# Kernel optimization log

Measured on AMD Instinct MI355X. Metric: run time of the kernel, lower is better.

The kernel has to match this reference:

```python
import jax, jax.numpy as jnp
import numpy as np

B = 131072    # batch of toy 2D points
H = 256       # effective hidden width (dims[1], = out_dims * group_card)
NB = 8        # n_blocks i-ResBlocks
NMID = 3      # middle layers: dims 2->256->256->256->256->2 => 1 in + 3 mid + 1 out
NPS = 5       # n_power_series terms for log-det trace estimator


def setup_inputs() -> dict:
    key = jax.random.key(0)
    ks = jax.random.split(key, 8)
    # small scales keep each g-net contractive (coeff<1 Lipschitz, as spectral norm would)
    x  = jax.random.normal(ks[0], (B, 2), jnp.float32)
    v  = jax.random.normal(ks[1], (B, 2), jnp.float32)  # Hutchinson probe (n_samples=1)
    Wi = jax.random.normal(ks[2], (NB, 2, H), jnp.float32) * 0.05
    bi = jax.random.normal(ks[3], (NB, H), jnp.float32) * 0.01
    Wm = jax.random.normal(ks[4], (NB, NMID, H, H), jnp.float32) * (0.05 / np.sqrt(H))
    bm = jax.random.normal(ks[5], (NB, NMID, H), jnp.float32) * 0.01
    Wo = jax.random.normal(ks[6], (NB, H, 2), jnp.float32) * (0.05 / np.sqrt(H))
    bo = jax.random.normal(ks[7], (NB, 2), jnp.float32) * 0.01
    return {"x": x, "v": v, "Wi": Wi, "bi": bi, "Wm": Wm, "bm": bm, "Wo": Wo, "bo": bo}


def _g(x, Wi, bi, Wm, bm, Wo, bo):
    # equivariant 3x3 convs on 1x1 spatial maps == channel-mixing linears;
    # build_nnet appends the activation after EVERY conv, including the last.
    h = jax.nn.relu(x @ Wi + bi)
    for j in range(Wm.shape[0]):
        h = jax.nn.relu(h @ Wm[j] + bm[j])
    return jax.nn.relu(h @ Wo + bo)


def _iresblock(x, v, Wi, bi, Wm, bm, Wo, bo):
    gfun = lambda xx: _g(xx, Wi, bi, Wm, bm, Wo, bo)
    gx = gfun(x)
    # log det(I + J_g) ~= sum_{k=1..n} (-1)^{k+1}/k * v^T J_g^k v  (power series, Hutchinson)
    w = v
    logdet = jnp.zeros((x.shape[0], 1), x.dtype)
    for k in range(1, NPS + 1):
        _, w = jax.jvp(gfun, (x,), (w,))          # w <- J_g @ w
        coef = ((-1.0) ** (k + 1)) / k
        logdet = logdet + coef * jnp.sum(w * v, axis=1, keepdims=True)
    return x + gx, logdet


def reference(x, v, Wi, bi, Wm, bm, Wo, bo):
    z = x
    delta_logp = jnp.zeros((x.shape[0], 1), x.dtype)  # SequentialFlow: logpx - logdet per block
    for b in range(NB):
        z, ld = _iresblock(z, v, Wi[b], bi[b], Wm[b], bm[b], Wo[b], bo[b])
        delta_logp = delta_logp - ld
    return z, delta_logp
```

## Files before the change

kernel.cpp:

```cpp
#include <hip/hip_runtime.h>
#include <hip/hip_bf16.h>

#define BATCH 131072
#define H 256
#define NBLK 8
#define NMID 3
#define MS 32
#define RT_N 6
#define NT 256

typedef __attribute__((ext_vector_type(8))) short short8;
typedef __attribute__((ext_vector_type(4))) float f32x4;

__device__ __forceinline__ unsigned pk2(float a, float b) {
    unsigned ua = __float_as_uint(a) + 0x8000u;
    unsigned ub = __float_as_uint(b) + 0x8000u;
    return __builtin_amdgcn_perm(ub, ua, 0x07060302u);
}
__device__ __forceinline__ unsigned short f2bf(float f) {
    return (unsigned short)((__float_as_uint(f) + 0x8000u) >> 16);
}

__global__ void pack_w_kernel(const float* __restrict__ Wm, unsigned short* __restrict__ Wp) {
    int o = blockIdx.x * blockDim.x + threadIdx.x;
    if (o >= NBLK * NMID * 8192) return;
    int lane  = o & 63;
    int T     = (o >> 6) & 15;
    int kk    = (o >> 10) & 7;
    int layer = o >> 13;
    int n  = (T >> 2) * 64 + (lane & 15) * 4 + (T & 3);
    int k0 = kk * 32 + (lane >> 4) * 8;
    const float* src = Wm + (size_t)layer * H * H;
    unsigned int w[4];
    #pragma unroll
    for (int jj = 0; jj < 4; ++jj)
        w[jj] = pk2(src[(size_t)(k0 + 2*jj) * H + n], src[(size_t)(k0 + 2*jj + 1) * H + n]);
    uint4 val; val.x = w[0]; val.y = w[1]; val.z = w[2]; val.w = w[3];
    ((uint4*)Wp)[o] = val;
}

__device__ __forceinline__ void epilogue_write(const f32x4 (&acc)[RT_N][4],
                                               const float* __restrict__ bias,
                                               unsigned short* __restrict__ Xs,
                                               int wave, int lane) {
    const int mcol = lane & 15, quad = lane >> 4;
    const int nb = wave * 64 + mcol * 4;
    const float4 bv = *(const float4*)(bias + nb);
    const int kkx = nb >> 5;
    const int qx  = (nb >> 3) & 3;
    const int jb  = nb & 7;
    #pragma unroll
    for (int g = 0; g < 2; ++g) {
        #pragma unroll
        for (int r = 0; r < 4; ++r) {
            float pre[4], hv[4], ta[4], tb[4];
            pre[0] = acc[g][0][r] + bv.x; pre[1] = acc[g][1][r] + bv.y;
            pre[2] = acc[g][2][r] + bv.z; pre[3] = acc[g][3][r] + bv.w;
            #pragma unroll
            for (int c = 0; c < 4; ++c) {
                bool mk = pre[c] > 0.0f;
                hv[c] = mk ? pre[c]        : 0.0f;
                ta[c] = mk ? acc[2+g][c][r] : 0.0f;
                tb[c] = mk ? acc[4+g][c][r] : 0.0f;
            }
            int rowm = quad * 4 + r;
            int le   = qx * 16 + rowm;
            int scl  = le ^ ((le >> 3) & 7);
            int e0   = (((g * 8 + kkx) * 64 + scl) * 8) + jb;
            uint2 ph; ph.x = pk2(hv[0], hv[1]); ph.y = pk2(hv[2], hv[3]);
            uint2 pa; pa.x = pk2(ta[0], ta[1]); pa.y = pk2(ta[2], ta[3]);
            uint2 pb; pb.x = pk2(tb[0], tb[1]); pb.y = pk2(tb[2], tb[3]);
            *(uint2*)(Xs + e0)          = ph;
            *(uint2*)(Xs + e0 + 8192)   = pa;
            *(uint2*)(Xs + e0 + 16384)  = pb;
        }
    }
}

__global__ __launch_bounds__(NT, 2)
void flow_kernel(const float* __restrict__ x, const float* __restrict__ v,
                 const float* __restrict__ Wi, const float* __restrict__ bi,
                 const float* __restrict__ bm, const float* __restrict__ Wo,
                 const float* __restrict__ bo,
                 const unsigned short* __restrict__ Wp,
                 float* __restrict__ out)
{
    __shared__ uint4 Xl4[RT_N * 8 * 64];
    __shared__ float zbuf[MS * 2];
    __shared__ float vbuf[MS * 2];

    unsigned short* Xs = (unsigned short*)Xl4;

    const int tid  = threadIdx.x;
    const int wave = tid >> 6;
    const int lane = tid & 63;
    const int mcol = lane & 15;
    const int quad = lane >> 4;
    const int s0   = blockIdx.x * MS;
    const int rl   = lane ^ ((lane >> 3) & 7);

    float dlp = 0.0f;
    if (tid < MS) {
        zbuf[tid*2+0] = x[(size_t)(s0+tid)*2+0];
        zbuf[tid*2+1] = x[(size_t)(s0+tid)*2+1];
        vbuf[tid*2+0] = v[(size_t)(s0+tid)*2+0];
        vbuf[tid*2+1] = v[(size_t)(s0+tid)*2+1];
    }
    __syncthreads();

    for (int b = 0; b < NBLK; ++b) {
        #pragma unroll
        for (int cc = 0; cc < 2; ++cc) {
            int c = cc * NT + tid;
            if (c < 384) {
                int rt = c >> 6, cl = c & 63;
                int l = cl ^ ((cl >> 3) & 7);
                int m = l & 15, q = l >> 4;
                int st = rt >> 1;
                uint4 pk = {0u, 0u, 0u, 0u};
                if (q == 0) {
                    if (st == 0) {
                        int s = ((rt & 1) << 4) | m;
                        pk.x = pk2(zbuf[s*2+0], zbuf[s*2+1]);
                    } else if (st == 1) pk.x = 0x00003F80u;
                    else                pk.x = 0x3F800000u;
                }
                Xl4[rt * 512 + cl] = pk;
            }
        }
        __syncthreads();

        const float* Wi0 = Wi + (size_t)b * 2 * H;
        const float* Wi1 = Wi0 + H;
        {
            short8 b0[4];
            #pragma unroll
            for (int ct = 0; ct < 4; ++ct) {
                short8 z = {0,0,0,0,0,0,0,0};
                if (lane < 16) {
                    int n = wave * 64 + lane * 4 + ct;
                    unsigned p = pk2(Wi0[n], Wi1[n]);
                    z[0] = (short)(p & 0xFFFFu);
                    z[1] = (short)(p >> 16);
                }
                b0[ct] = z;
            }
            f32x4 acc[RT_N][4];
            #pragma unroll
            for (int rt = 0; rt < RT_N; ++rt)
                #pragma unroll
                for (int ct = 0; ct < 4; ++ct)
                    acc[rt][ct] = (f32x4){0.f, 0.f, 0.f, 0.f};
            #pragma unroll
            for (int rt = 0; rt < RT_N; ++rt) {
                short8 af = ((const short8*)Xl4)[(rt * 8) * 64 + rl];
                #pragma unroll
                for (int ct = 0; ct < 4; ++ct)
                    acc[rt][ct] = __builtin_amdgcn_mfma_f32_16x16x32_bf16(af, b0[ct], acc[rt][ct], 0, 0, 0);
            }
            __syncthreads();
            epilogue_write(acc, bi + (size_t)b * H, Xs, wave, lane);
            __syncthreads();
        }

        for (int li = 0; li < NMID; ++li) {
            const int layer = b * NMID + li;
            const short8* Bp  = ((const short8*)Wp) + (size_t)layer * 8192;
            const float* bias = bm + (size_t)layer * H;

            f32x4 acc[RT_N][4];
            #pragma unroll
            for (int rt = 0; rt < RT_N; ++rt)
                #pragma unroll
                for (int ct = 0; ct < 4; ++ct)
                    acc[rt][ct] = (f32x4){0.f, 0.f, 0.f, 0.f};

            #pragma unroll
            for (int kk = 0; kk < 8; ++kk) {
                short8 bf[4];
                #pragma unroll
                for (int ct = 0; ct < 4; ++ct)
                    bf[ct] = Bp[(kk*16 + wave*4 + ct)*64 + lane];
                #pragma unroll
                for (int rt = 0; rt < RT_N; ++rt) {
                    short8 af = ((const short8*)Xl4)[(rt*8 + kk)*64 + rl];
                    #pragma unroll
                    for (int ct = 0; ct < 4; ++ct)
                        acc[rt][ct] = __builtin_amdgcn_mfma_f32_16x16x32_bf16(af, bf[ct], acc[rt][ct], 0, 0, 0);
                }
            }
            __syncthreads();
            epilogue_write(acc, bias, Xs, wave, lane);
            __syncthreads();
        }

        const float* Wob = Wo + (size_t)b * H * 2;
        const float* bob = bo + (size_t)b * 2;
        {
            short8 b4[2];
            #pragma unroll
            for (int kki = 0; kki < 2; ++kki) {
                short8 z = {0,0,0,0,0,0,0,0};
                if (mcol < 2) {
                    int kb = (wave * 2 + kki) * 32 + quad * 8;
                    #pragma unroll
                    for (int jj = 0; jj < 4; ++jj) {
                        unsigned p = pk2(Wob[(kb + 2*jj) * 2 + mcol], Wob[(kb + 2*jj + 1) * 2 + mcol]);
                        z[2*jj]   = (short)(p & 0xFFFFu);
                        z[2*jj+1] = (short)(p >> 16);
                    }
                }
                b4[kki] = z;
            }
            f32x4 accL[RT_N];
            #pragma unroll
            for (int rt = 0; rt < RT_N; ++rt) accL[rt] = (f32x4){0.f, 0.f, 0.f, 0.f};
            #pragma unroll
            for (int rt = 0; rt < RT_N; ++rt) {
                short8 a0 = ((const short8*)Xl4)[(rt*8 + wave*2    )*64 + rl];
                accL[rt] = __builtin_amdgcn_mfma_f32_16x16x32_bf16(a0, b4[0], accL[rt], 0, 0, 0);
                short8 a1 = ((const short8*)Xl4)[(rt*8 + wave*2 + 1)*64 + rl];
                accL[rt] = __builtin_amdgcn_mfma_f32_16x16x32_bf16(a1, b4[1], accL[rt], 0, 0, 0);
            }
            __syncthreads();
            float* part = (float*)Xl4;
            if (mcol < 2) {
                #pragma unroll
                for (int rt = 0; rt < RT_N; ++rt)
                    #pragma unroll
                    for (int r = 0; r < 4; ++r)
                        part[((rt*16 + quad*4 + r)*2 + mcol)*4 + wave] = accL[rt][r];
            }
            __syncthreads();
            float* res = part + 768;
            if (tid < 192) {
                float4 p4 = ((const float4*)part)[tid];
                res[tid] = p4.x + p4.y + p4.z + p4.w;
            }
            __syncthreads();
            if (tid < MS) {
                int g = tid >> 4, row = tid & 15;
                int base = (g * 16 + row) * 2;
                float SH0 = res[base], SH1 = res[base + 1];
                float SA0 = res[base + 64], SA1 = res[base + 65];
                float SB0 = res[base + 128], SB1 = res[base + 129];
                float pre0 = SH0 + bob[0], pre1 = SH1 + bob[1];
                bool  m0 = pre0 > 0.f,     m1 = pre1 > 0.f;
                float gx0 = m0 ? pre0 : 0.f, gx1 = m1 ? pre1 : 0.f;
                float J00 = m0 ? SA0 : 0.f;
                float J01 = m0 ? SB0 : 0.f;
                float J10 = m1 ? SA1 : 0.f;
                float J11 = m1 ? SB1 : 0.f;
                float v0 = vbuf[tid*2+0], v1 = vbuf[tid*2+1];
                float w0 = v0, w1 = v1, ld = 0.f;
                const float coef[5] = {1.f, -0.5f, 1.f/3.f, -0.25f, 0.2f};
                #pragma unroll
                for (int k = 0; k < 5; ++k) {
                    float nw0 = fmaf(J00, w0, J01 * w1);
                    float nw1 = fmaf(J10, w0, J11 * w1);
                    w0 = nw0; w1 = nw1;
                    ld = fmaf(coef[k], fmaf(w0, v0, w1 * v1), ld);
                }
                zbuf[tid*2+0] += gx0;
                zbuf[tid*2+1] += gx1;
                dlp -= ld;
            }
        }
        __syncthreads();
    }

    if (tid < MS) {
        out[(size_t)(s0+tid)*2+0] = zbuf[tid*2+0];
        out[(size_t)(s0+tid)*2+1] = zbuf[tid*2+1];
        out[(size_t)2*BATCH + s0 + tid] = dlp;
    }
}

extern "C" void kernel_launch(void* const* d_in, const int* in_sizes, int n_in,
                              void* d_out, int out_size, void* d_ws, size_t ws_size,
                              hipStream_t stream) {
    const float* x  = (const float*)d_in[0];
    const float* v  = (const float*)d_in[1];
    const float* Wi = (const float*)d_in[2];
    const float* bi = (const float*)d_in[3];
    const float* Wm = (const float*)d_in[4];
    const float* bm = (const float*)d_in[5];
    const float* Wo = (const float*)d_in[6];
    const float* bo = (const float*)d_in[7];
    unsigned short* Wp = (unsigned short*)d_ws;

    int nchunks = NBLK * NMID * 8192;
    pack_w_kernel<<<(nchunks + 255) / 256, 256, 0, stream>>>(Wm, Wp);
    flow_kernel<<<BATCH / MS, NT, 0, stream>>>(x, v, Wi, bi, bm, Wo, bo, Wp, (float*)d_out);
}
```

Before: 1.261 ms.

## Split hidden columns across eight waves and build input-layer fragments in registers

Doubles the block size to 512 threads, so each wave computes 32 instead of 64 output columns per layer, halving per-wave MFMA work and accumulator registers. The weight packing layout and epilogue indexing change to match, and the reduction of the output layer now sums eight wave partials. The first layer's A fragments are now built directly from zbuf in registers instead of being staged through LDS, which removes one barrier per block. The middle-layer epilogue math runs before the barrier so it can overlap with other waves. The cost is more barrier participants and a larger cross-wave reduction, in exchange for lower register pressure and more waves in flight to hide latency.

```diff
diff --git a/kernel.cpp b/kernel.cpp
--- a/kernel.cpp
+++ b/kernel.cpp
@@ -7,7 +7,8 @@
 #define NMID 3
 #define MS 32
 #define RT_N 6
-#define NT 256
+#define NT 512
+#define CT_N 2
 
 typedef __attribute__((ext_vector_type(8))) short short8;
 typedef __attribute__((ext_vector_type(4))) float f32x4;
@@ -16,9 +17,6 @@
     unsigned ua = __float_as_uint(a) + 0x8000u;
     unsigned ub = __float_as_uint(b) + 0x8000u;
     return __builtin_amdgcn_perm(ub, ua, 0x07060302u);
-}
-__device__ __forceinline__ unsigned short f2bf(float f) {
-    return (unsigned short)((__float_as_uint(f) + 0x8000u) >> 16);
 }
 
 __global__ void pack_w_kernel(const float* __restrict__ Wm, unsigned short* __restrict__ Wp) {
@@ -28,7 +26,7 @@
     int T     = (o >> 6) & 15;
     int kk    = (o >> 10) & 7;
     int layer = o >> 13;
-    int n  = (T >> 2) * 64 + (lane & 15) * 4 + (T & 3);
+    int n  = (T >> 1) * 32 + (lane & 15) * 2 + (T & 1);
     int k0 = kk * 32 + (lane >> 4) * 8;
     const float* src = Wm + (size_t)layer * H * H;
     unsigned int w[4];
@@ -39,45 +37,44 @@
     ((uint4*)Wp)[o] = val;
 }
 
-__device__ __forceinline__ void epilogue_write(const f32x4 (&acc)[RT_N][4],
-                                               const float* __restrict__ bias,
-                                               unsigned short* __restrict__ Xs,
-                                               int wave, int lane) {
-    const int mcol = lane & 15, quad = lane >> 4;
-    const int nb = wave * 64 + mcol * 4;
-    const float4 bv = *(const float4*)(bias + nb);
-    const int kkx = nb >> 5;
-    const int qx  = (nb >> 3) & 3;
-    const int jb  = nb & 7;
+struct Packs { unsigned ph[2][4]; unsigned pa[2][4]; unsigned pb[2][4]; };
+
+__device__ __forceinline__ void epi_compute(const f32x4 (&acc)[RT_N][CT_N],
+                                            const float2 bv, Packs& p) {
     #pragma unroll
     for (int g = 0; g < 2; ++g) {
         #pragma unroll
         for (int r = 0; r < 4; ++r) {
-            float pre[4], hv[4], ta[4], tb[4];
-            pre[0] = acc[g][0][r] + bv.x; pre[1] = acc[g][1][r] + bv.y;
-            pre[2] = acc[g][2][r] + bv.z; pre[3] = acc[g][3][r] + bv.w;
-            #pragma unroll
-            for (int c = 0; c < 4; ++c) {
-                bool mk = pre[c] > 0.0f;
-                hv[c] = mk ? pre[c]        : 0.0f;
-                ta[c] = mk ? acc[2+g][c][r] : 0.0f;
-                tb[c] = mk ? acc[4+g][c][r] : 0.0f;
-            }
-            int rowm = quad * 4 + r;
-            int le   = qx * 16 + rowm;
-            int scl  = le ^ ((le >> 3) & 7);
-            int e0   = (((g * 8 + kkx) * 64 + scl) * 8) + jb;
-            uint2 ph; ph.x = pk2(hv[0], hv[1]); ph.y = pk2(hv[2], hv[3]);
-            uint2 pa; pa.x = pk2(ta[0], ta[1]); pa.y = pk2(ta[2], ta[3]);
-            uint2 pb; pb.x = pk2(tb[0], tb[1]); pb.y = pk2(tb[2], tb[3]);
-            *(uint2*)(Xs + e0)          = ph;
-            *(uint2*)(Xs + e0 + 8192)   = pa;
-            *(uint2*)(Xs + e0 + 16384)  = pb;
-        }
-    }
-}
-
-__global__ __launch_bounds__(NT, 2)
+            float c0 = acc[g][0][r] + bv.x;
+            float c1 = acc[g][1][r] + bv.y;
+            bool m0 = c0 > 0.0f, m1 = c1 > 0.0f;
+            p.ph[g][r] = pk2(m0 ? c0 : 0.0f,             m1 ? c1 : 0.0f);
+            p.pa[g][r] = pk2(m0 ? acc[2+g][0][r] : 0.0f, m1 ? acc[2+g][1][r] : 0.0f);
+            p.pb[g][r] = pk2(m0 ? acc[4+g][0][r] : 0.0f, m1 ? acc[4+g][1][r] : 0.0f);
+        }
+    }
+}
+
+__device__ __forceinline__ void epi_store(const Packs& p, unsigned short* __restrict__ Xs,
+                                          int wave, int lane) {
+    const int mcol = lane & 15, quad = lane >> 4;
+    const int qx = (mcol >> 2) & 3;
+    const int jb = (mcol & 3) * 2;
+    #pragma unroll
+    for (int g = 0; g < 2; ++g) {
+        #pragma unroll
+        for (int r = 0; r < 4; ++r) {
+            int le  = qx * 16 + quad * 4 + r;
+            int scl = le ^ ((le >> 3) & 7);
+            int e0  = ((g * 8 + wave) * 64 + scl) * 8 + jb;
+            *(unsigned*)(Xs + e0)         = p.ph[g][r];
+            *(unsigned*)(Xs + e0 + 8192)  = p.pa[g][r];
+            *(unsigned*)(Xs + e0 + 16384) = p.pb[g][r];
+        }
+    }
+}
+
+__global__ __launch_bounds__(NT, 4)
 void flow_kernel(const float* __restrict__ x, const float* __restrict__ v,
                  const float* __restrict__ Wi, const float* __restrict__ bi,
                  const float* __restrict__ bm, const float* __restrict__ Wo,
@@ -109,118 +106,102 @@
     __syncthreads();
 
     for (int b = 0; b < NBLK; ++b) {
-        #pragma unroll
-        for (int cc = 0; cc < 2; ++cc) {
-            int c = cc * NT + tid;
-            if (c < 384) {
-                int rt = c >> 6, cl = c & 63;
-                int l = cl ^ ((cl >> 3) & 7);
-                int m = l & 15, q = l >> 4;
-                int st = rt >> 1;
-                uint4 pk = {0u, 0u, 0u, 0u};
-                if (q == 0) {
-                    if (st == 0) {
-                        int s = ((rt & 1) << 4) | m;
-                        pk.x = pk2(zbuf[s*2+0], zbuf[s*2+1]);
-                    } else if (st == 1) pk.x = 0x00003F80u;
-                    else                pk.x = 0x3F800000u;
-                }
-                Xl4[rt * 512 + cl] = pk;
-            }
-        }
-        __syncthreads();
-
-        const float* Wi0 = Wi + (size_t)b * 2 * H;
-        const float* Wi1 = Wi0 + H;
         {
-            short8 b0[4];
-            #pragma unroll
-            for (int ct = 0; ct < 4; ++ct) {
+            const float* Wi0 = Wi + (size_t)b * 2 * H;
+            const float* Wi1 = Wi0 + H;
+            short8 b0[CT_N];
+            #pragma unroll
+            for (int ct = 0; ct < CT_N; ++ct) {
                 short8 z = {0,0,0,0,0,0,0,0};
-                if (lane < 16) {
-                    int n = wave * 64 + lane * 4 + ct;
+                if (quad == 0) {
+                    int n = wave * 32 + mcol * 2 + ct;
                     unsigned p = pk2(Wi0[n], Wi1[n]);
                     z[0] = (short)(p & 0xFFFFu);
                     z[1] = (short)(p >> 16);
                 }
                 b0[ct] = z;
             }
-            f32x4 acc[RT_N][4];
+            f32x4 acc[RT_N][CT_N];
             #pragma unroll
             for (int rt = 0; rt < RT_N; ++rt)
                 #pragma unroll
-                for (int ct = 0; ct < 4; ++ct)
+                for (int ct = 0; ct < CT_N; ++ct)
                     acc[rt][ct] = (f32x4){0.f, 0.f, 0.f, 0.f};
             #pragma unroll
             for (int rt = 0; rt < RT_N; ++rt) {
-                short8 af = ((const short8*)Xl4)[(rt * 8) * 64 + rl];
-                #pragma unroll
-                for (int ct = 0; ct < 4; ++ct)
+                short8 af = {0,0,0,0,0,0,0,0};
+                int st = rt >> 1;
+                if (quad == 0) {
+                    if (st == 0) {
+                        int s = (rt & 1) * 16 + mcol;
+                        unsigned p = pk2(zbuf[s*2+0], zbuf[s*2+1]);
+                        af[0] = (short)(p & 0xFFFFu);
+                        af[1] = (short)(p >> 16);
+                    } else if (st == 1) af[0] = (short)0x3F80;
+                    else                af[1] = (short)0x3F80;
+                }
+                #pragma unroll
+                for (int ct = 0; ct < CT_N; ++ct)
                     acc[rt][ct] = __builtin_amdgcn_mfma_f32_16x16x32_bf16(af, b0[ct], acc[rt][ct], 0, 0, 0);
             }
-            __syncthreads();
-            epilogue_write(acc, bi + (size_t)b * H, Xs, wave, lane);
+            Packs p;
+            epi_compute(acc, *(const float2*)(bi + (size_t)b * H + wave*32 + mcol*2), p);
+            epi_store(p, Xs, wave, lane);
             __syncthreads();
         }
 
         for (int li = 0; li < NMID; ++li) {
             const int layer = b * NMID + li;
-            const short8* Bp  = ((const short8*)Wp) + (size_t)layer * 8192;
-            const float* bias = bm + (size_t)layer * H;
-
-            f32x4 acc[RT_N][4];
+            const short8* Bp = ((const short8*)Wp) + (size_t)layer * 8192;
+
+            f32x4 acc[RT_N][CT_N];
             #pragma unroll
             for (int rt = 0; rt < RT_N; ++rt)
                 #pragma unroll
-                for (int ct = 0; ct < 4; ++ct)
+                for (int ct = 0; ct < CT_N; ++ct)
                     acc[rt][ct] = (f32x4){0.f, 0.f, 0.f, 0.f};
 
             #pragma unroll
             for (int kk = 0; kk < 8; ++kk) {
-                short8 bf[4];
-                #pragma unroll
-                for (int ct = 0; ct < 4; ++ct)
-                    bf[ct] = Bp[(kk*16 + wave*4 + ct)*64 + lane];
+                short8 bf[CT_N];
+                #pragma unroll
+                for (int ct = 0; ct < CT_N; ++ct)
+                    bf[ct] = Bp[(kk*16 + wave*2 + ct)*64 + lane];
                 #pragma unroll
                 for (int rt = 0; rt < RT_N; ++rt) {
                     short8 af = ((const short8*)Xl4)[(rt*8 + kk)*64 + rl];
                     #pragma unroll
-                    for (int ct = 0; ct < 4; ++ct)
+                    for (int ct = 0; ct < CT_N; ++ct)
                         acc[rt][ct] = __builtin_amdgcn_mfma_f32_16x16x32_bf16(af, bf[ct], acc[rt][ct], 0, 0, 0);
                 }
             }
-            __syncthreads();
-            epilogue_write(acc, bias, Xs, wave, lane);
-            __syncthreads();
-        }
-
-        const float* Wob = Wo + (size_t)b * H * 2;
-        const float* bob = bo + (size_t)b * 2;
+            Packs p;
+            epi_compute(acc, *(const float2*)(bm + (size_t)layer * H + wave*32 + mcol*2), p);
+            __syncthreads();
+            epi_store(p, Xs, wave, lane);
+            __syncthreads();
+        }
+
         {
-            short8 b4[2];
-            #pragma unroll
-            for (int kki = 0; kki < 2; ++kki) {
-                short8 z = {0,0,0,0,0,0,0,0};
-                if (mcol < 2) {
-                    int kb = (wave * 2 + kki) * 32 + quad * 8;
-                    #pragma unroll
-                    for (int jj = 0; jj < 4; ++jj) {
-                        unsigned p = pk2(Wob[(kb + 2*jj) * 2 + mcol], Wob[(kb + 2*jj + 1) * 2 + mcol]);
-                        z[2*jj]   = (short)(p & 0xFFFFu);
-                        z[2*jj+1] = (short)(p >> 16);
-                    }
-                }
-                b4[kki] = z;
+            const float* Wob = Wo + (size_t)b * H * 2;
+            const float* bob = bo + (size_t)b * 2;
+            short8 b4 = {0,0,0,0,0,0,0,0};
+            if (mcol < 2) {
+                int kb = wave * 32 + quad * 8;
+                #pragma unroll
+                for (int jj = 0; jj < 4; ++jj) {
+                    unsigned p = pk2(Wob[(kb + 2*jj) * 2 + mcol], Wob[(kb + 2*jj + 1) * 2 + mcol]);
+                    b4[2*jj]   = (short)(p & 0xFFFFu);
+                    b4[2*jj+1] = (short)(p >> 16);
+                }
             }
             f32x4 accL[RT_N];
             #pragma unroll
             for (int rt = 0; rt < RT_N; ++rt) accL[rt] = (f32x4){0.f, 0.f, 0.f, 0.f};
             #pragma unroll
             for (int rt = 0; rt < RT_N; ++rt) {
-                short8 a0 = ((const short8*)Xl4)[(rt*8 + wave*2    )*64 + rl];
-                accL[rt] = __builtin_amdgcn_mfma_f32_16x16x32_bf16(a0, b4[0], accL[rt], 0, 0, 0);
-                short8 a1 = ((const short8*)Xl4)[(rt*8 + wave*2 + 1)*64 + rl];
-                accL[rt] = __builtin_amdgcn_mfma_f32_16x16x32_bf16(a1, b4[1], accL[rt], 0, 0, 0);
+                short8 af = ((const short8*)Xl4)[(rt*8 + wave)*64 + rl];
+                accL[rt] = __builtin_amdgcn_mfma_f32_16x16x32_bf16(af, b4, accL[rt], 0, 0, 0);
             }
             __syncthreads();
             float* part = (float*)Xl4;
@@ -229,21 +210,20 @@
                 for (int rt = 0; rt < RT_N; ++rt)
                     #pragma unroll
                     for (int r = 0; r < 4; ++r)
-                        part[((rt*16 + quad*4 + r)*2 + mcol)*4 + wave] = accL[rt][r];
-            }
-            __syncthreads();
-            float* res = part + 768;
+                        part[((rt*16 + quad*4 + r)*2 + mcol)*8 + wave] = accL[rt][r];
+            }
+            __syncthreads();
+            float* res = part + 1536;
             if (tid < 192) {
-                float4 p4 = ((const float4*)part)[tid];
-                res[tid] = p4.x + p4.y + p4.z + p4.w;
+                float4 p0 = ((const float4*)part)[tid*2];
+                float4 p1 = ((const float4*)part)[tid*2+1];
+                res[tid] = (p0.x + p0.y + p0.z + p0.w) + (p1.x + p1.y + p1.z + p1.w);
             }
             __syncthreads();
             if (tid < MS) {
-                int g = tid >> 4, row = tid & 15;
-                int base = (g * 16 + row) * 2;
-                float SH0 = res[base], SH1 = res[base + 1];
-                float SA0 = res[base + 64], SA1 = res[base + 65];
-                float SB0 = res[base + 128], SB1 = res[base + 129];
+                float SH0 = res[tid*2],       SH1 = res[tid*2+1];
+                float SA0 = res[64 + tid*2],  SA1 = res[65 + tid*2];
+                float SB0 = res[128 + tid*2], SB1 = res[129 + tid*2];
                 float pre0 = SH0 + bob[0], pre1 = SH1 + bob[1];
                 bool  m0 = pre0 > 0.f,     m1 = pre1 > 0.f;
                 float gx0 = m0 ? pre0 : 0.f, gx1 = m1 ? pre1 : 0.f;
@@ -265,8 +245,8 @@
                 zbuf[tid*2+1] += gx1;
                 dlp -= ld;
             }
-        }
-        __syncthreads();
+            __syncthreads();
+        }
     }
 
     if (tid < MS) {
```

New measurement: 1.560 ms. 1.24x slower.
